# Performance work log

Hardware: AMD Instinct MI355X
Metric: run time of the kernel (lower is better)

## Reference

```python
import jax, jax.numpy as jnp
import numpy as np

B, H, W, C = 8, 64, 64, 512
CK, CV = C // 8, C // 2  # 64, 256


def maxpool2x2(x):
    # x: [B, H, W, C] -> [B, H//2, W//2, C], 2x2 max pool, stride 2 (keras MaxPooling2D default)
    b, h, w, c = x.shape
    return x.reshape(b, h // 2, 2, w // 2, 2, c).max(axis=(2, 4))


def setup_inputs() -> dict:
    key = jax.random.key(0)
    ks = jax.random.split(key, 6)
    wscale = 0.02
    return {
        "x": jax.random.normal(ks[0], (B, H, W, C), dtype=jnp.float32),
        "w_theta": jax.random.normal(ks[1], (C, CK), dtype=jnp.float32) * wscale,
        "w_phi": jax.random.normal(ks[2], (C, CK), dtype=jnp.float32) * wscale,
        "w_g": jax.random.normal(ks[3], (C, CV), dtype=jnp.float32) * wscale,
        "w_o": jax.random.normal(ks[4], (CV, C), dtype=jnp.float32) * wscale,
        "gamma": jax.random.normal(ks[5], (1,), dtype=jnp.float32),
    }


def reference(x, w_theta, w_phi, w_g, w_o, gamma):
    b, h, w, c = x.shape
    hw = h * w
    # theta: 1x1 conv -> [B, HW, C//8]
    theta = jnp.einsum('bhwc,ck->bhwk', x, w_theta).reshape(b, hw, -1)
    # phi: 1x1 conv + 2x2 maxpool -> [B, HW//4, C//8]
    phi = maxpool2x2(jnp.einsum('bhwc,ck->bhwk', x, w_phi)).reshape(b, hw // 4, -1)
    # attention: [B, HW, HW//4], softmax over last axis
    attn = jax.nn.softmax(jnp.einsum('bqk,bpk->bqp', theta, phi), axis=-1)
    # g: 1x1 conv + 2x2 maxpool -> [B, HW//4, C//2]
    g = maxpool2x2(jnp.einsum('bhwc,cv->bhwv', x, w_g)).reshape(b, hw // 4, -1)
    # attn_g: [B, HW, C//2] -> [B, H, W, C//2] -> 1x1 conv -> [B, H, W, C]
    attn_g = jnp.einsum('bqp,bpv->bqv', attn, g).reshape(b, h, w, -1)
    attn_g = jnp.einsum('bhwv,vc->bhwc', attn_g, w_o)
    return x + gamma * attn_g
```

## Files before the change

kernel.cpp:

```cpp
#include <hip/hip_runtime.h>
#include <hip/hip_bf16.h>
#include <cstddef>
#include <cstdint>


typedef __attribute__((ext_vector_type(8))) short short8;
typedef __attribute__((ext_vector_type(4))) float float4v;

namespace {
constexpr int kB = 8, kC = 512, kCK = 64, kCV = 256, kHW = 4096, kP = 1024;
constexpr int kNP = 384;
}

__device__ __forceinline__ short f2b(float f) {
  __hip_bfloat16 h = __float2bfloat16(f);
  return __builtin_bit_cast(short, h);
}

__device__ __forceinline__ void gll16(const void* g, void* l) {
  __builtin_amdgcn_global_load_lds((uint32_t __attribute__((address_space(1)))*)g,
                                   (uint32_t __attribute__((address_space(3)))*)l,
                                   16, 0, 0);
}

__device__ __forceinline__ float4v mfma16(short8 a, short8 b, float4v c) {
  return __builtin_amdgcn_mfma_f32_16x16x32_bf16(a, b, c, 0, 0, 0);
}

enum { EPI_BF16 = 0, EPI_RESID = 2 };

template <int BM, int BN, int WR, int WC, int EPI>
__global__ __launch_bounds__(256) void gemm_bt(
    const __hip_bfloat16* __restrict__ A, const __hip_bfloat16* __restrict__ B,
    void* __restrict__ C, int M, int N, int K,
    const float* __restrict__ xres, const float* __restrict__ gamma) {
  constexpr int TM = BM / WR, TN = BN / WC;
  constexpr int NMT = TM / 16, NNT = TN / 16;
  __shared__ __hip_bfloat16 As[BM * 64];
  __shared__ __hip_bfloat16 Bs[BN * 64];
  const int tid = threadIdx.x;
  const int wid = tid >> 6;
  const int lane = tid & 63;
  const int m = lane & 15, quad = lane >> 4;
  const int row0 = blockIdx.x * BM;
  const int col0 = blockIdx.y * BN;
  const int wm = (wid / WC) * TM;
  const int wn = (wid % WC) * TN;

  float4v acc[NMT][NNT] = {};

  const int srow = tid >> 3;
  const int scol = (tid & 7) * 8;
  const __hip_bfloat16* aptr = A + (size_t)(row0 + srow) * K + scol;
  const __hip_bfloat16* bptr = B + (size_t)(col0 + srow) * K + scol;

  for (int kc = 0; kc < K; kc += 64) {
#pragma unroll
    for (int u = 0; u < BM / 32; ++u)
      gll16(aptr + (size_t)u * 32 * K + kc, &As[(u * 32 + wid * 8) * 64]);
#pragma unroll
    for (int u = 0; u < BN / 32; ++u)
      gll16(bptr + (size_t)u * 32 * K + kc, &Bs[(u * 32 + wid * 8) * 64]);
    __syncthreads();
#pragma unroll
    for (int kk = 0; kk < 64; kk += 32) {
      short8 af[NMT], bfr[NNT];
#pragma unroll
      for (int i = 0; i < NMT; ++i)
        af[i] = *(const short8*)&As[(wm + i * 16 + m) * 64 + kk + quad * 8];
#pragma unroll
      for (int j = 0; j < NNT; ++j)
        bfr[j] = *(const short8*)&Bs[(wn + j * 16 + m) * 64 + kk + quad * 8];
#pragma unroll
      for (int i = 0; i < NMT; ++i)
#pragma unroll
        for (int j = 0; j < NNT; ++j)
          acc[i][j] = mfma16(af[i], bfr[j], acc[i][j]);
    }
    __syncthreads();
  }
#pragma unroll
  for (int i = 0; i < NMT; ++i) {
#pragma unroll
    for (int j = 0; j < NNT; ++j) {
      const int cc = col0 + wn + j * 16 + m;
      const int rb = row0 + wm + i * 16 + quad * 4;
#pragma unroll
      for (int r = 0; r < 4; ++r) {
        const size_t idx = (size_t)(rb + r) * N + cc;
        if constexpr (EPI == EPI_BF16) {
          ((__hip_bfloat16*)C)[idx] = __float2bfloat16(acc[i][j][r]);
        } else {
          ((float*)C)[idx] = xres[idx] + gamma[0] * acc[i][j][r];
        }
      }
    }
  }
}

__global__ __launch_bounds__(256) void k_cast_x(const float* __restrict__ x,
                                                __hip_bfloat16* __restrict__ xb) {
  const int i = blockIdx.x * 256 + threadIdx.x;
  const float4v* xv = (const float4v*)x;
  float4v v0 = xv[i * 2], v1 = xv[i * 2 + 1];
  short8 o;
  o[0] = f2b(v0[0]); o[1] = f2b(v0[1]); o[2] = f2b(v0[2]); o[3] = f2b(v0[3]);
  o[4] = f2b(v1[0]); o[5] = f2b(v1[1]); o[6] = f2b(v1[2]); o[7] = f2b(v1[3]);
  ((short8*)xb)[i] = o;
}

__global__ __launch_bounds__(256) void k_pack_w(
    const float* __restrict__ wt, const float* __restrict__ wphi,
    const float* __restrict__ wg, const float* __restrict__ wo,
    __hip_bfloat16* __restrict__ wAll, __hip_bfloat16* __restrict__ woT) {
  int idx = blockIdx.x * 256 + threadIdx.x;
  if (idx < 196608) {
    int n = idx >> 9, k = idx & 511;
    float v = (n < 64) ? wt[k * 64 + n]
            : (n < 128) ? wphi[k * 64 + (n - 64)]
                        : wg[k * 256 + (n - 128)];
    wAll[idx] = __float2bfloat16(v);
  } else {
    int t = idx - 196608;
    int n = t >> 8, k = t & 255;
    woT[t] = __float2bfloat16(wo[k * 512 + n]);
  }
}

__global__ __launch_bounds__(256) void k_pool_phi(const __hip_bfloat16* __restrict__ pg,
                                                  __hip_bfloat16* __restrict__ phi_p) {
  int idx = blockIdx.x * 256 + threadIdx.x;
  int c = idx & 63;
  int p = (idx >> 6) & 1023;
  int b = idx >> 16;
  int ph = p >> 5, pw = p & 31;
  size_t base = ((size_t)b * 4096 + ph * 128 + pw * 2) * kNP + 64 + c;
  float v0 = __bfloat162float(pg[base]);
  float v1 = __bfloat162float(pg[base + kNP]);
  float v2 = __bfloat162float(pg[base + kNP * 64]);
  float v3 = __bfloat162float(pg[base + kNP * 64 + kNP]);
  phi_p[idx] = __float2bfloat16(fmaxf(fmaxf(v0, v1), fmaxf(v2, v3)));
}

__global__ __launch_bounds__(256) void k_pool_gT(const __hip_bfloat16* __restrict__ pg,
                                                 __hip_bfloat16* __restrict__ gT) {
  __shared__ __hip_bfloat16 t[64][65];
  const int p0 = blockIdx.x * 64, v0 = blockIdx.y * 64, b = blockIdx.z;
#pragma unroll
  for (int it = 0; it < 16; ++it) {
    int li = it * 256 + threadIdx.x;
    int pp = li >> 6, v = li & 63;
    int p = p0 + pp;
    int ph = p >> 5, pw = p & 31;
    size_t base = ((size_t)b * 4096 + ph * 128 + pw * 2) * kNP + 128 + v0 + v;
    float m = fmaxf(
        fmaxf(__bfloat162float(pg[base]), __bfloat162float(pg[base + kNP])),
        fmaxf(__bfloat162float(pg[base + kNP * 64]), __bfloat162float(pg[base + kNP * 64 + kNP])));
    t[pp][v] = __float2bfloat16(m);
  }
  __syncthreads();
#pragma unroll
  for (int it = 0; it < 16; ++it) {
    int li = it * 256 + threadIdx.x;
    int v = li >> 6, p = li & 63;
    gT[((size_t)b * 256 + v0 + v) * 1024 + p0 + p] = t[p][v];
  }
}

__global__ __launch_bounds__(512) void k_fattn(
    const __hip_bfloat16* __restrict__ pgf,
    const __hip_bfloat16* __restrict__ phip,
    const __hip_bfloat16* __restrict__ gT,
    __hip_bfloat16* __restrict__ O) {
  __shared__ __align__(16) char smem[65536 + 8704 + 1024 + 128];
  __hip_bfloat16* Ks = (__hip_bfloat16*)smem;
  __hip_bfloat16* Gs = (__hip_bfloat16*)smem;
  __hip_bfloat16* Qs = (__hip_bfloat16*)(smem + 65536);
  __hip_bfloat16* Ps = (__hip_bfloat16*)(smem + 65536);
  float* pred = (float*)(smem + 65536 + 8704);
  float* rowstat = (float*)(smem + 65536 + 8704 + 1024);

  const int tid = threadIdx.x;
  const int wid = tid >> 6;
  const int lane = tid & 63;
  const int m = lane & 15, quad = lane >> 4;
  const int b = blockIdx.y;
  const int q0 = blockIdx.x * 32;

  if (wid < 4) {
    const __hip_bfloat16* src =
        pgf + ((size_t)(b * kHW + q0 + wid * 8 + (lane >> 3))) * kNP + (lane & 7) * 8;
    gll16(src, Qs + wid * 8 * 64);
  }

  float4v sc[2][8] = {};
  const __hip_bfloat16* phb = phip + (size_t)b * kP * 64;
  for (int c = 0; c < 4; ++c) {
#pragma unroll
    for (int u = 0; u < 4; ++u)
      gll16(phb + (size_t)(c * 256 + u * 64 + (tid >> 3)) * 64 + (tid & 7) * 8,
            Ks + (u * 64 + wid * 8) * 64);
    __syncthreads();
#pragma unroll
    for (int kk = 0; kk < 64; kk += 32) {
      short8 a[2], bb[2];
#pragma unroll
      for (int i = 0; i < 2; ++i)
        a[i] = *(const short8*)&Qs[(i * 16 + m) * 64 + kk + quad * 8];
#pragma unroll
      for (int j = 0; j < 2; ++j)
        bb[j] = *(const short8*)&Ks[(wid * 32 + j * 16 + m) * 64 + kk + quad * 8];
#pragma unroll
      for (int i = 0; i < 2; ++i)
#pragma unroll
        for (int j = 0; j < 2; ++j)
          sc[i][c * 2 + j] = mfma16(a[i], bb[j], sc[i][c * 2 + j]);
    }
    __syncthreads();
  }

  float mx[2][4];
#pragma unroll
  for (int i = 0; i < 2; ++i)
#pragma unroll
    for (int r = 0; r < 4; ++r) {
      float v = sc[i][0][r];
#pragma unroll
      for (int s = 1; s < 8; ++s) v = fmaxf(v, sc[i][s][r]);
#pragma unroll
      for (int d = 1; d < 16; d <<= 1) v = fmaxf(v, __shfl_xor(v, d));
      mx[i][r] = v;
    }
  if (m == 0) {
#pragma unroll
    for (int i = 0; i < 2; ++i)
#pragma unroll
      for (int r = 0; r < 4; ++r) pred[(i * 16 + quad * 4 + r) * 8 + wid] = mx[i][r];
  }
  __syncthreads();
  if (tid < 32) {
    float v = pred[tid * 8];
#pragma unroll
    for (int w = 1; w < 8; ++w) v = fmaxf(v, pred[tid * 8 + w]);
    rowstat[tid] = v;
  }
  __syncthreads();
  float sm[2][4];
#pragma unroll
  for (int i = 0; i < 2; ++i)
#pragma unroll
    for (int r = 0; r < 4; ++r) {
      const float rm = rowstat[i * 16 + quad * 4 + r];
      float s = 0.f;
#pragma unroll
      for (int ss = 0; ss < 8; ++ss) {
        float e = __expf(sc[i][ss][r] - rm);
        sc[i][ss][r] = e;
        s += e;
      }
#pragma unroll
      for (int d = 1; d < 16; d <<= 1) s += __shfl_xor(s, d);
      sm[i][r] = s;
    }
  __syncthreads();
  if (m == 0) {
#pragma unroll
    for (int i = 0; i < 2; ++i)
#pragma unroll
      for (int r = 0; r < 4; ++r) pred[(i * 16 + quad * 4 + r) * 8 + wid] = sm[i][r];
  }
  __syncthreads();
  if (tid < 32) {
    float s = 0.f;
#pragma unroll
    for (int w = 0; w < 8; ++w) s += pred[tid * 8 + w];
    rowstat[tid] = 1.f / s;
  }

  float4v oc[2][2] = {};
  const __hip_bfloat16* gb = gT + (size_t)b * kCV * kP;
  for (int c2 = 0; c2 < 8; ++c2) {
#pragma unroll
    for (int u = 0; u < 8; ++u)
      gll16(gb + (size_t)(u * 32 + (tid >> 4)) * kP + c2 * 128 + (lane & 15) * 8,
            Gs + (u * 32 + wid * 4) * 128);
    if ((wid >> 2) == (c2 & 1)) {
      const int lc0 = (wid & 3) * 32;
      const int sbase = (c2 >> 1) * 2;
#pragma unroll
      for (int i = 0; i < 2; ++i)
#pragma unroll
        for (int j = 0; j < 2; ++j)
#pragma unroll
          for (int r = 0; r < 4; ++r)
            Ps[(i * 16 + quad * 4 + r) * 136 + lc0 + j * 16 + m] =
                __float2bfloat16(sc[i][sbase + j][r]);
    }
    __syncthreads();
#pragma unroll
    for (int kk = 0; kk < 128; kk += 32) {
      short8 a[2], bb[2];
#pragma unroll
      for (int i = 0; i < 2; ++i)
        a[i] = *(const short8*)&Ps[(i * 16 + m) * 136 + kk + quad * 8];
#pragma unroll
      for (int j = 0; j < 2; ++j)
        bb[j] = *(const short8*)&Gs[(wid * 32 + j * 16 + m) * 128 + kk + quad * 8];
#pragma unroll
      for (int i = 0; i < 2; ++i)
#pragma unroll
        for (int j = 0; j < 2; ++j) oc[i][j] = mfma16(a[i], bb[j], oc[i][j]);
    }
    __syncthreads();
  }
#pragma unroll
  for (int i = 0; i < 2; ++i)
#pragma unroll
    for (int j = 0; j < 2; ++j)
#pragma unroll
      for (int r = 0; r < 4; ++r) {
        const int row = i * 16 + quad * 4 + r;
        O[((size_t)b * kHW + q0 + row) * kCV + wid * 32 + j * 16 + m] =
            __float2bfloat16(oc[i][j][r] * rowstat[row]);
      }
}

extern "C" void kernel_launch(void* const* d_in, const int* in_sizes, int n_in,
                              void* d_out, int out_size, void* d_ws, size_t ws_size,
                              hipStream_t stream) {
  (void)in_sizes; (void)n_in; (void)out_size; (void)ws_size;
  const float* x     = (const float*)d_in[0];
  const float* wt    = (const float*)d_in[1];
  const float* wphi  = (const float*)d_in[2];
  const float* wg    = (const float*)d_in[3];
  const float* wo    = (const float*)d_in[4];
  const float* wo_g  = (const float*)d_in[5];
  float* out = (float*)d_out;

  char* ws = (char*)d_ws;
  __hip_bfloat16* xbf  = (__hip_bfloat16*)(ws);
  __hip_bfloat16* wAll = (__hip_bfloat16*)(ws + 33554432);
  __hip_bfloat16* woT  = (__hip_bfloat16*)(ws + 33947648);
  __hip_bfloat16* pgf  = (__hip_bfloat16*)(ws + 34209792);
  __hip_bfloat16* phip = (__hip_bfloat16*)(ws + 59375616);
  __hip_bfloat16* gT   = (__hip_bfloat16*)(ws + 60424192);
  __hip_bfloat16* O    = xbf;

  k_cast_x<<<8192, 256, 0, stream>>>(x, xbf);
  k_pack_w<<<1280, 256, 0, stream>>>(wt, wphi, wg, wo, wAll, woT);
  gemm_bt<128, 128, 2, 2, EPI_BF16><<<dim3(256, 3), 256, 0, stream>>>(
      xbf, wAll, pgf, 32768, kNP, 512, nullptr, nullptr);
  k_pool_phi<<<2048, 256, 0, stream>>>(pgf, phip);
  k_pool_gT<<<dim3(16, 4, 8), 256, 0, stream>>>(pgf, gT);
  k_fattn<<<dim3(kHW / 32, kB), 512, 0, stream>>>(pgf, phip, gT, O);
  gemm_bt<128, 128, 2, 2, EPI_RESID><<<dim3(256, 4), 256, 0, stream>>>(
      O, woT, out, 32768, kC, kCV, x, wo_g);
}
```

Baseline: 263.1 us.

## Fuse x cast into projection GEMM, add XOR-swizzled LDS and double buffering

Removes the separate fp32-to-bf16 cast kernel: the projection GEMM now loads fp32 x tiles straight into LDS and converts them in registers, computing all 384 output columns per block so x is read once. All GEMM-style kernels (projection, attention and output) switch to XOR-swizzled LDS layouts to avoid bank conflicts. The attention and output GEMM loops are double-buffered so the next tile's global-to-LDS loads overlap the current MFMAs. The attention kernel also gets an occupancy hint in its launch bounds. The cost is much higher register pressure from the 2x12 accumulators in the projection kernel, and the fp32 LDS staging doubles A-tile traffic.

Result: faster. 257.6 us (-2.1%).

```diff
diff --git a/kernel.cpp b/kernel.cpp
--- a/kernel.cpp
+++ b/kernel.cpp
@@ -12,101 +12,16 @@
 constexpr int kNP = 384;
 }
 
-__device__ __forceinline__ short f2b(float f) {
-  __hip_bfloat16 h = __float2bfloat16(f);
-  return __builtin_bit_cast(short, h);
-}
-
 __device__ __forceinline__ void gll16(const void* g, void* l) {
   __builtin_amdgcn_global_load_lds((uint32_t __attribute__((address_space(1)))*)g,
                                    (uint32_t __attribute__((address_space(3)))*)l,
                                    16, 0, 0);
 }
-
 __device__ __forceinline__ float4v mfma16(short8 a, short8 b, float4v c) {
   return __builtin_amdgcn_mfma_f32_16x16x32_bf16(a, b, c, 0, 0, 0);
 }
-
-enum { EPI_BF16 = 0, EPI_RESID = 2 };
-
-template <int BM, int BN, int WR, int WC, int EPI>
-__global__ __launch_bounds__(256) void gemm_bt(
-    const __hip_bfloat16* __restrict__ A, const __hip_bfloat16* __restrict__ B,
-    void* __restrict__ C, int M, int N, int K,
-    const float* __restrict__ xres, const float* __restrict__ gamma) {
-  constexpr int TM = BM / WR, TN = BN / WC;
-  constexpr int NMT = TM / 16, NNT = TN / 16;
-  __shared__ __hip_bfloat16 As[BM * 64];
-  __shared__ __hip_bfloat16 Bs[BN * 64];
-  const int tid = threadIdx.x;
-  const int wid = tid >> 6;
-  const int lane = tid & 63;
-  const int m = lane & 15, quad = lane >> 4;
-  const int row0 = blockIdx.x * BM;
-  const int col0 = blockIdx.y * BN;
-  const int wm = (wid / WC) * TM;
-  const int wn = (wid % WC) * TN;
-
-  float4v acc[NMT][NNT] = {};
-
-  const int srow = tid >> 3;
-  const int scol = (tid & 7) * 8;
-  const __hip_bfloat16* aptr = A + (size_t)(row0 + srow) * K + scol;
-  const __hip_bfloat16* bptr = B + (size_t)(col0 + srow) * K + scol;
-
-  for (int kc = 0; kc < K; kc += 64) {
-#pragma unroll
-    for (int u = 0; u < BM / 32; ++u)
-      gll16(aptr + (size_t)u * 32 * K + kc, &As[(u * 32 + wid * 8) * 64]);
-#pragma unroll
-    for (int u = 0; u < BN / 32; ++u)
-      gll16(bptr + (size_t)u * 32 * K + kc, &Bs[(u * 32 + wid * 8) * 64]);
-    __syncthreads();
-#pragma unroll
-    for (int kk = 0; kk < 64; kk += 32) {
-      short8 af[NMT], bfr[NNT];
-#pragma unroll
-      for (int i = 0; i < NMT; ++i)
-        af[i] = *(const short8*)&As[(wm + i * 16 + m) * 64 + kk + quad * 8];
-#pragma unroll
-      for (int j = 0; j < NNT; ++j)
-        bfr[j] = *(const short8*)&Bs[(wn + j * 16 + m) * 64 + kk + quad * 8];
-#pragma unroll
-      for (int i = 0; i < NMT; ++i)
-#pragma unroll
-        for (int j = 0; j < NNT; ++j)
-          acc[i][j] = mfma16(af[i], bfr[j], acc[i][j]);
-    }
-    __syncthreads();
-  }
-#pragma unroll
-  for (int i = 0; i < NMT; ++i) {
-#pragma unroll
-    for (int j = 0; j < NNT; ++j) {
-      const int cc = col0 + wn + j * 16 + m;
-      const int rb = row0 + wm + i * 16 + quad * 4;
-#pragma unroll
-      for (int r = 0; r < 4; ++r) {
-        const size_t idx = (size_t)(rb + r) * N + cc;
-        if constexpr (EPI == EPI_BF16) {
-          ((__hip_bfloat16*)C)[idx] = __float2bfloat16(acc[i][j][r]);
-        } else {
-          ((float*)C)[idx] = xres[idx] + gamma[0] * acc[i][j][r];
-        }
-      }
-    }
-  }
-}
-
-__global__ __launch_bounds__(256) void k_cast_x(const float* __restrict__ x,
-                                                __hip_bfloat16* __restrict__ xb) {
-  const int i = blockIdx.x * 256 + threadIdx.x;
-  const float4v* xv = (const float4v*)x;
-  float4v v0 = xv[i * 2], v1 = xv[i * 2 + 1];
-  short8 o;
-  o[0] = f2b(v0[0]); o[1] = f2b(v0[1]); o[2] = f2b(v0[2]); o[3] = f2b(v0[3]);
-  o[4] = f2b(v1[0]); o[5] = f2b(v1[1]); o[6] = f2b(v1[2]); o[7] = f2b(v1[3]);
-  ((short8*)xb)[i] = o;
+__device__ __forceinline__ const short8* fragp(const char* tile, int row, int oct) {
+  return (const short8*)(tile + row * 128 + ((oct ^ (row & 7)) * 16));
 }
 
 __global__ __launch_bounds__(256) void k_pack_w(
@@ -127,6 +42,73 @@
   }
 }
 
+__global__ __launch_bounds__(256) void k_proj(const float* __restrict__ x,
+                                              const __hip_bfloat16* __restrict__ wAll,
+                                              __hip_bfloat16* __restrict__ pgf) {
+  __shared__ __align__(16) char smem[16384 + 49152];
+  char* As = smem;
+  char* Bs = smem + 16384;
+  const int tid = threadIdx.x, wid = tid >> 6, lane = tid & 63;
+  const int m = lane & 15, quad = lane >> 4;
+  const int row0 = blockIdx.x * 64;
+  const int wm = (wid >> 1) * 32, wn = (wid & 1) * 192;
+  float4v acc[2][12] = {};
+  for (int kc = 0; kc < 512; kc += 64) {
+#pragma unroll
+    for (int u = 0; u < 4; ++u) {
+      const int r0 = (wid * 4 + u) * 4;
+      const int row = r0 + (lane >> 4);
+      const int sqg = (lane & 15) ^ (row & 15);
+      gll16(x + (size_t)(row0 + row) * 512 + kc + sqg * 4, As + r0 * 256);
+    }
+#pragma unroll
+    for (int u = 0; u < 12; ++u) {
+      const int r0 = (wid * 12 + u) * 8;
+      const int row = r0 + (lane >> 3);
+      const int og = (lane & 7) ^ (row & 7);
+      gll16(wAll + (size_t)row * 512 + kc + og * 8, Bs + r0 * 128);
+    }
+    __syncthreads();
+#pragma unroll
+    for (int kk = 0; kk < 64; kk += 32) {
+      short8 af[2];
+#pragma unroll
+      for (int i = 0; i < 2; ++i) {
+        const int row = wm + i * 16 + m;
+        const int sq0 = (kk >> 2) + quad * 2;
+        float4v lo = *(const float4v*)(As + row * 256 + ((sq0 ^ m) * 16));
+        float4v hi = *(const float4v*)(As + row * 256 + (((sq0 + 1) ^ m) * 16));
+        short8 a;
+        a[0] = __builtin_bit_cast(short, __float2bfloat16(lo[0]));
+        a[1] = __builtin_bit_cast(short, __float2bfloat16(lo[1]));
+        a[2] = __builtin_bit_cast(short, __float2bfloat16(lo[2]));
+        a[3] = __builtin_bit_cast(short, __float2bfloat16(lo[3]));
+        a[4] = __builtin_bit_cast(short, __float2bfloat16(hi[0]));
+        a[5] = __builtin_bit_cast(short, __float2bfloat16(hi[1]));
+        a[6] = __builtin_bit_cast(short, __float2bfloat16(hi[2]));
+        a[7] = __builtin_bit_cast(short, __float2bfloat16(hi[3]));
+        af[i] = a;
+      }
+      const int oct = (kk >> 3) + quad;
+#pragma unroll
+      for (int j = 0; j < 12; ++j) {
+        short8 bf = *fragp(Bs, wn + j * 16 + m, oct);
+#pragma unroll
+        for (int i = 0; i < 2; ++i) acc[i][j] = mfma16(af[i], bf, acc[i][j]);
+      }
+    }
+    __syncthreads();
+  }
+#pragma unroll
+  for (int i = 0; i < 2; ++i)
+#pragma unroll
+    for (int j = 0; j < 12; ++j)
+#pragma unroll
+      for (int r = 0; r < 4; ++r)
+        pgf[(size_t)(row0 + wm + i * 16 + quad * 4 + r) * 384 + wn + j * 16 + m] =
+            __float2bfloat16(acc[i][j][r]);
+}
+
 __global__ __launch_bounds__(256) void k_pool_phi(const __hip_bfloat16* __restrict__ pg,
                                                   __hip_bfloat16* __restrict__ phi_p) {
   int idx = blockIdx.x * 256 + threadIdx.x;
@@ -153,10 +135,10 @@
     int p = p0 + pp;
     int ph = p >> 5, pw = p & 31;
     size_t base = ((size_t)b * 4096 + ph * 128 + pw * 2) * kNP + 128 + v0 + v;
-    float m = fmaxf(
+    float mv = fmaxf(
         fmaxf(__bfloat162float(pg[base]), __bfloat162float(pg[base + kNP])),
         fmaxf(__bfloat162float(pg[base + kNP * 64]), __bfloat162float(pg[base + kNP * 64 + kNP])));
-    t[pp][v] = __float2bfloat16(m);
+    t[pp][v] = __float2bfloat16(mv);
   }
   __syncthreads();
 #pragma unroll
@@ -167,54 +149,56 @@
   }
 }
 
-__global__ __launch_bounds__(512) void k_fattn(
+__global__ __launch_bounds__(512, 4) void k_fattn(
     const __hip_bfloat16* __restrict__ pgf,
     const __hip_bfloat16* __restrict__ phip,
     const __hip_bfloat16* __restrict__ gT,
     __hip_bfloat16* __restrict__ O) {
-  __shared__ __align__(16) char smem[65536 + 8704 + 1024 + 128];
-  __hip_bfloat16* Ks = (__hip_bfloat16*)smem;
-  __hip_bfloat16* Gs = (__hip_bfloat16*)smem;
-  __hip_bfloat16* Qs = (__hip_bfloat16*)(smem + 65536);
-  __hip_bfloat16* Ps = (__hip_bfloat16*)(smem + 65536);
-  float* pred = (float*)(smem + 65536 + 8704);
-  float* rowstat = (float*)(smem + 65536 + 8704 + 1024);
-
-  const int tid = threadIdx.x;
-  const int wid = tid >> 6;
-  const int lane = tid & 63;
+  __shared__ __align__(16) char smem[65536 + 8192 + 1024 + 128];
+  char* KG = smem;
+  char* PQ = smem + 65536;
+  float* pred = (float*)(smem + 65536 + 8192);
+  float* rowstat = (float*)(smem + 65536 + 8192 + 1024);
+
+  const int tid = threadIdx.x, wid = tid >> 6, lane = tid & 63;
   const int m = lane & 15, quad = lane >> 4;
-  const int b = blockIdx.y;
-  const int q0 = blockIdx.x * 32;
+  const int b = blockIdx.y, q0 = blockIdx.x * 32;
 
   if (wid < 4) {
-    const __hip_bfloat16* src =
-        pgf + ((size_t)(b * kHW + q0 + wid * 8 + (lane >> 3))) * kNP + (lane & 7) * 8;
-    gll16(src, Qs + wid * 8 * 64);
-  }
+    const int row = wid * 8 + (lane >> 3);
+    const int og = (lane & 7) ^ (row & 7);
+    gll16(pgf + (size_t)(b * kHW + q0 + row) * kNP + og * 8, PQ + wid * 8 * 128);
+  }
+  const __hip_bfloat16* phb = phip + (size_t)b * kP * 64;
+  auto stageK = [&](int c, int buf) {
+#pragma unroll
+    for (int u = 0; u < 4; ++u) {
+      const int r0 = wid * 32 + u * 8;
+      const int row = r0 + (lane >> 3);
+      const int og = (lane & 7) ^ (row & 7);
+      gll16(phb + (size_t)(c * 256 + row) * 64 + og * 8, KG + buf * 32768 + r0 * 128);
+    }
+  };
+  stageK(0, 0);
+  __syncthreads();
 
   float4v sc[2][8] = {};
-  const __hip_bfloat16* phb = phip + (size_t)b * kP * 64;
+#pragma unroll
   for (int c = 0; c < 4; ++c) {
-#pragma unroll
-    for (int u = 0; u < 4; ++u)
-      gll16(phb + (size_t)(c * 256 + u * 64 + (tid >> 3)) * 64 + (tid & 7) * 8,
-            Ks + (u * 64 + wid * 8) * 64);
-    __syncthreads();
+    if (c < 3) stageK(c + 1, (c + 1) & 1);
+    const char* Kb = KG + (c & 1) * 32768;
 #pragma unroll
     for (int kk = 0; kk < 64; kk += 32) {
+      const int oct = (kk >> 3) + quad;
       short8 a[2], bb[2];
 #pragma unroll
+      for (int i = 0; i < 2; ++i) a[i] = *fragp(PQ, i * 16 + m, oct);
+#pragma unroll
+      for (int j = 0; j < 2; ++j) bb[j] = *fragp(Kb, wid * 32 + j * 16 + m, oct);
+#pragma unroll
       for (int i = 0; i < 2; ++i)
-        a[i] = *(const short8*)&Qs[(i * 16 + m) * 64 + kk + quad * 8];
-#pragma unroll
-      for (int j = 0; j < 2; ++j)
-        bb[j] = *(const short8*)&Ks[(wid * 32 + j * 16 + m) * 64 + kk + quad * 8];
-#pragma unroll
-      for (int i = 0; i < 2; ++i)
-#pragma unroll
-        for (int j = 0; j < 2; ++j)
-          sc[i][c * 2 + j] = mfma16(a[i], bb[j], sc[i][c * 2 + j]);
+#pragma unroll
+        for (int j = 0; j < 2; ++j) sc[i][c * 2 + j] = mfma16(a[i], bb[j], sc[i][c * 2 + j]);
     }
     __syncthreads();
   }
@@ -277,35 +261,55 @@
     rowstat[tid] = 1.f / s;
   }
 
+  const __hip_bfloat16* gb = gT + (size_t)b * kCV * kP;
+  auto stageG = [&](int cp, int buf) {
+#pragma unroll
+    for (int u = 0; u < 4; ++u) {
+      const int r0 = wid * 32 + u * 8;
+      const int row = r0 + (lane >> 3);
+      const int og = (lane & 7) ^ (row & 7);
+      gll16(gb + (size_t)row * kP + cp * 64 + og * 8, KG + buf * 32768 + r0 * 128);
+    }
+  };
+  auto writeP = [&](int cp, int pbuf) {
+    if ((wid >> 1) == (cp & 3)) {
+      const int c = cp >> 2;
+#pragma unroll
+      for (int i = 0; i < 2; ++i)
+#pragma unroll
+        for (int jl = 0; jl < 2; ++jl) {
+          const int pl = (wid & 1) * 32 + jl * 16 + m;
+#pragma unroll
+          for (int r = 0; r < 4; ++r) {
+            const int row = i * 16 + quad * 4 + r;
+            *(__hip_bfloat16*)(PQ + pbuf * 4096 + row * 128 +
+                               (((pl >> 3) ^ (row & 7)) * 16) + (pl & 7) * 2) =
+                __float2bfloat16(sc[i][c * 2 + jl][r]);
+          }
+        }
+    }
+  };
+  writeP(0, 0);
+  stageG(0, 0);
+  __syncthreads();
+
   float4v oc[2][2] = {};
-  const __hip_bfloat16* gb = gT + (size_t)b * kCV * kP;
-  for (int c2 = 0; c2 < 8; ++c2) {
-#pragma unroll
-    for (int u = 0; u < 8; ++u)
-      gll16(gb + (size_t)(u * 32 + (tid >> 4)) * kP + c2 * 128 + (lane & 15) * 8,
-            Gs + (u * 32 + wid * 4) * 128);
-    if ((wid >> 2) == (c2 & 1)) {
-      const int lc0 = (wid & 3) * 32;
-      const int sbase = (c2 >> 1) * 2;
-#pragma unroll
-      for (int i = 0; i < 2; ++i)
-#pragma unroll
-        for (int j = 0; j < 2; ++j)
-#pragma unroll
-          for (int r = 0; r < 4; ++r)
-            Ps[(i * 16 + quad * 4 + r) * 136 + lc0 + j * 16 + m] =
-                __float2bfloat16(sc[i][sbase + j][r]);
-    }
-    __syncthreads();
-#pragma unroll
-    for (int kk = 0; kk < 128; kk += 32) {
+#pragma unroll
+  for (int cp = 0; cp < 16; ++cp) {
+    if (cp < 15) {
+      stageG(cp + 1, (cp + 1) & 1);
+      writeP(cp + 1, (cp + 1) & 1);
+    }
+    const char* Gb = KG + (cp & 1) * 32768;
+    const char* Pb = PQ + (cp & 1) * 4096;
+#pragma unroll
+    for (int kk = 0; kk < 64; kk += 32) {
+      const int oct = (kk >> 3) + quad;
       short8 a[2], bb[2];
 #pragma unroll
-      for (int i = 0; i < 2; ++i)
-        a[i] = *(const short8*)&Ps[(i * 16 + m) * 136 + kk + quad * 8];
-#pragma unroll
-      for (int j = 0; j < 2; ++j)
-        bb[j] = *(const short8*)&Gs[(wid * 32 + j * 16 + m) * 128 + kk + quad * 8];
+      for (int i = 0; i < 2; ++i) a[i] = *fragp(Pb, i * 16 + m, oct);
+#pragma unroll
+      for (int j = 0; j < 2; ++j) bb[j] = *fragp(Gb, wid * 32 + j * 16 + m, oct);
 #pragma unroll
       for (int i = 0; i < 2; ++i)
 #pragma unroll
@@ -323,6 +327,66 @@
         O[((size_t)b * kHW + q0 + row) * kCV + wid * 32 + j * 16 + m] =
             __float2bfloat16(oc[i][j][r] * rowstat[row]);
       }
+}
+
+__global__ __launch_bounds__(256) void k_out(const __hip_bfloat16* __restrict__ A,
+                                             const __hip_bfloat16* __restrict__ Bw,
+                                             const float* __restrict__ x,
+                                             const float* __restrict__ gamma,
+                                             float* __restrict__ out) {
+  __shared__ __align__(16) char smem[4 * 16384];
+  const int tid = threadIdx.x, wid = tid >> 6, lane = tid & 63;
+  const int m = lane & 15, quad = lane >> 4;
+  const int row0 = blockIdx.x * 128, col0 = blockIdx.y * 128;
+  const int wm = (wid >> 1) * 64, wn = (wid & 1) * 64;
+  float4v acc[4][4] = {};
+  auto stage = [&](int t, int buf) {
+    const int kc = t * 64;
+#pragma unroll
+    for (int u = 0; u < 4; ++u) {
+      const int r0 = (wid * 4 + u) * 8;
+      const int row = r0 + (lane >> 3);
+      const int og = (lane & 7) ^ (row & 7);
+      gll16(A + (size_t)(row0 + row) * 256 + kc + og * 8, smem + buf * 16384 + r0 * 128);
+      gll16(Bw + (size_t)(col0 + row) * 256 + kc + og * 8,
+            smem + 32768 + buf * 16384 + r0 * 128);
+    }
+  };
+  stage(0, 0);
+  __syncthreads();
+#pragma unroll
+  for (int t = 0; t < 4; ++t) {
+    if (t < 3) stage(t + 1, (t + 1) & 1);
+    const char* Ab = smem + (t & 1) * 16384;
+    const char* Bb = smem + 32768 + (t & 1) * 16384;
+#pragma unroll
+    for (int kk = 0; kk < 64; kk += 32) {
+      const int oct = (kk >> 3) + quad;
+      short8 af[4], bf[4];
+#pragma unroll
+      for (int i = 0; i < 4; ++i) af[i] = *fragp(Ab, wm + i * 16 + m, oct);
+#pragma unroll
+      for (int j = 0; j < 4; ++j) bf[j] = *fragp(Bb, wn + j * 16 + m, oct);
+#pragma unroll
+      for (int i = 0; i < 4; ++i)
+#pragma unroll
+        for (int j = 0; j < 4; ++j) acc[i][j] = mfma16(af[i], bf[j], acc[i][j]);
+    }
+    __syncthreads();
+  }
+  const float g = gamma[0];
+#pragma unroll
+  for (int i = 0; i < 4; ++i)
+#pragma unroll
+    for (int j = 0; j < 4; ++j) {
+      const int cc = col0 + wn + j * 16 + m;
+      const int rb = row0 + wm + i * 16 + quad * 4;
+#pragma unroll
+      for (int r = 0; r < 4; ++r) {
+        const size_t idx = (size_t)(rb + r) * 512 + cc;
+        out[idx] = x[idx] + g * acc[i][j][r];
+      }
+    }
 }
 
 extern "C" void kernel_launch(void* const* d_in, const int* in_sizes, int n_in,
@@ -334,25 +398,21 @@
   const float* wphi  = (const float*)d_in[2];
   const float* wg    = (const float*)d_in[3];
   const float* wo    = (const float*)d_in[4];
-  const float* wo_g  = (const float*)d_in[5];
+  const float* gamma = (const float*)d_in[5];
   float* out = (float*)d_out;
 
   char* ws = (char*)d_ws;
-  __hip_bfloat16* xbf  = (__hip_bfloat16*)(ws);
-  __hip_bfloat16* wAll = (__hip_bfloat16*)(ws + 33554432);
-  __hip_bfloat16* woT  = (__hip_bfloat16*)(ws + 33947648);
-  __hip_bfloat16* pgf  = (__hip_bfloat16*)(ws + 34209792);
-  __hip_bfloat16* phip = (__hip_bfloat16*)(ws + 59375616);
-  __hip_bfloat16* gT   = (__hip_bfloat16*)(ws + 60424192);
-  __hip_bfloat16* O    = xbf;
-
-  k_cast_x<<<8192, 256, 0, stream>>>(x, xbf);
+  __hip_bfloat16* wAll = (__hip_bfloat16*)(ws);
+  __hip_bfloat16* woT  = (__hip_bfloat16*)(ws + 393216);
+  __hip_bfloat16* pgf  = (__hip_bfloat16*)(ws + 655360);
+  __hip_bfloat16* phip = (__hip_bfloat16*)(ws + 25821184);
+  __hip_bfloat16* gT   = (__hip_bfloat16*)(ws + 26869760);
+  __hip_bfloat16* O    = (__hip_bfloat16*)(ws + 31064064);
+
   k_pack_w<<<1280, 256, 0, stream>>>(wt, wphi, wg, wo, wAll, woT);
-  gemm_bt<128, 128, 2, 2, EPI_BF16><<<dim3(256, 3), 256, 0, stream>>>(
-      xbf, wAll, pgf, 32768, kNP, 512, nullptr, nullptr);
+  k_proj<<<512, 256, 0, stream>>>(x, wAll, pgf);
   k_pool_phi<<<2048, 256, 0, stream>>>(pgf, phip);
   k_pool_gT<<<dim3(16, 4, 8), 256, 0, stream>>>(pgf, gT);
   k_fattn<<<dim3(kHW / 32, kB), 512, 0, stream>>>(pgf, phip, gT, O);
-  gemm_bt<128, 128, 2, 2, EPI_RESID><<<dim3(256, 4), 256, 0, stream>>>(
-      O, woT, out, 32768, kC, kCV, x, wo_g);
-}
+  k_out<<<dim3(256, 4), 256, 0, stream>>>(O, woT, x, gamma, out);
+}
```
